# Optimization experiments

Hardware: AMD Instinct MI355X
Metric: run time of the kernel (lower is better)

Reference implementation:

```python
import jax, jax.numpy as jnp
import numpy as np

# model geometry (matches init_kwargs cfg)
D = 768        # D_EMB
PATCH = 16
T = 8192
N = T // PATCH # 512 patch tokens
H = 12         # heads
HD = D // H    # 64 head dim
NL = 6         # layers
DFF = 4 * D
B = 8
LN_EPS = 1e-5


def setup_inputs() -> dict:
    key = jax.random.key(0)
    ks = iter(jax.random.split(key, 32))
    def g(shape, scale=0.02):
        return jax.random.normal(next(ks), shape, jnp.float32) * scale
    return dict(
        x=jax.random.normal(next(ks), (B, T), jnp.float32),
        pp_w=g((D, PATCH)), pp_b=jnp.zeros((D,), jnp.float32),
        pe=g((N, D)),
        ln1_g=jnp.ones((NL, D), jnp.float32), ln1_b=jnp.zeros((NL, D), jnp.float32),
        qkv_w=g((NL, 3 * D, D)), out_w=g((NL, D, D)),
        ln2_g=jnp.ones((NL, D), jnp.float32), ln2_b=jnp.zeros((NL, D), jnp.float32),
        fc1_w=g((NL, DFF, D)), fc2_w=g((NL, D, DFF)),
        lnf_g=jnp.ones((D,), jnp.float32), lnf_b=jnp.zeros((D,), jnp.float32),
        h1_w=g((D // 2, D)), h1_b=jnp.zeros((D // 2,), jnp.float32),
        h2_w=g((2, D // 2)), h2_b=jnp.zeros((2,), jnp.float32),
    )


def _ln(x, g, b):
    m = x.mean(-1, keepdims=True)
    v = ((x - m) ** 2).mean(-1, keepdims=True)
    return (x - m) / jnp.sqrt(v + LN_EPS) * g + b


def reference(x, pp_w, pp_b, pe, ln1_g, ln1_b, qkv_w, out_w,
              ln2_g, ln2_b, fc1_w, fc2_w, lnf_g, lnf_b,
              h1_w, h1_b, h2_w, h2_b):
    Bx = x.shape[0]
    # patch embed: [B, N, PATCH] @ W^T + b -> [B, N, D]
    z = jnp.einsum('bnp,dp->bnd', x[:, :N * PATCH].reshape(Bx, N, PATCH), pp_w) + pp_b
    z = z + pe  # positional embedding (arange indexes whole table)
    mask = jnp.tril(jnp.ones((N, N), dtype=bool))
    for i in range(NL):
        # --- attention (manual causal softmax, dropout=eval/no-op) ---
        h = _ln(z, ln1_g[i], ln1_b[i])
        qkv = jnp.einsum('bnd,ed->bne', h, qkv_w[i])            # [B,N,3D]
        qkv = qkv.reshape(Bx, N, 3, H, HD).transpose(2, 0, 3, 1, 4)
        q, k, v = qkv[0], qkv[1], qkv[2]                         # [B,H,N,HD]
        s = jnp.einsum('bhld,bhmd->bhlm', q, k) / np.sqrt(HD)
        s = jnp.where(mask, s, -jnp.inf)
        a = jax.nn.softmax(s, axis=-1)
        o = jnp.einsum('bhlm,bhmd->bhld', a, v)
        o = o.transpose(0, 2, 1, 3).reshape(Bx, N, D)
        z = z + jnp.einsum('bnd,ed->bne', o, out_w[i])
        # --- FFN (exact gelu, matching F.gelu default) ---
        h = _ln(z, ln2_g[i], ln2_b[i])
        f = jax.nn.gelu(jnp.einsum('bnd,fd->bnf', h, fc1_w[i]), approximate=False)
        z = z + jnp.einsum('bnf,df->bnd', f, fc2_w[i])
    enc = _ln(z, lnf_g, lnf_b).mean(axis=1)                      # [B, D]
    y = jax.nn.relu(enc @ h1_w.T + h1_b)
    return y @ h2_w.T + h2_b                                     # [B, 2]
```

## Files before the change

kernel.cpp:

```cpp
#include <hip/hip_runtime.h>
#include <hip/hip_bf16.h>
#include <math.h>

#define D_EMB 768
#define NPATCH 16
#define NTOK 512
#define NHEAD 12
#define HDIM 64
#define NLAYER 6
#define DFF 3072
#define BATCH 8
#define MTOK (BATCH * NTOK)

typedef __attribute__((ext_vector_type(8))) short bf16x8;
typedef __attribute__((ext_vector_type(4))) float f32x4;

__device__ __forceinline__ float bf2f(ushort s) {
    unsigned u = ((unsigned)s) << 16;
    return __builtin_bit_cast(float, u);
}
__device__ __forceinline__ ushort f2bf(float f) {
    unsigned u = __builtin_bit_cast(unsigned, f);
    unsigned r = (u + 0x7FFFu + ((u >> 16) & 1u)) >> 16;
    return (ushort)r;
}

__global__ __launch_bounds__(256)
void f2bf_kernel(const float* __restrict__ in, ushort* __restrict__ out, int n4)
{
    int i = blockIdx.x * 256 + threadIdx.x;
    if (i >= n4) return;
    float4 v = *(const float4*)(in + (size_t)i * 4);
    ushort4 o;
    o.x = f2bf(v.x); o.y = f2bf(v.y); o.z = f2bf(v.z); o.w = f2bf(v.w);
    *(ushort4*)(out + (size_t)i * 4) = o;
}

__global__ __launch_bounds__(256)
void patch_embed_kernel(const float* __restrict__ x, const float* __restrict__ pw,
                        const float* __restrict__ pb, const float* __restrict__ pe,
                        float* __restrict__ z)
{
    int bn = blockIdx.x;
    int b = bn >> 9, n = bn & 511;
    __shared__ float xs[NPATCH];
    int t = threadIdx.x;
    if (t < NPATCH) xs[t] = x[(size_t)b * 8192 + n * NPATCH + t];
    __syncthreads();
    for (int d = t; d < D_EMB; d += 256) {
        float acc = pb[d] + pe[(size_t)n * D_EMB + d];
        const float* w = pw + (size_t)d * NPATCH;
        #pragma unroll
        for (int p = 0; p < NPATCH; ++p) acc += xs[p] * w[p];
        z[(size_t)bn * D_EMB + d] = acc;
    }
}

__device__ __forceinline__ float block_reduce_sum_256(float v)
{
    __shared__ float lds[4];
    #pragma unroll
    for (int o = 32; o > 0; o >>= 1) v += __shfl_xor(v, o);
    int lane = threadIdx.x & 63, wid = threadIdx.x >> 6;
    __syncthreads();
    if (lane == 0) lds[wid] = v;
    __syncthreads();
    return lds[0] + lds[1] + lds[2] + lds[3];
}

__device__ __forceinline__ void store_val(float* p, float v)  { *p = v; }
__device__ __forceinline__ void store_val(ushort* p, float v) { *p = f2bf(v); }

template<typename OT>
__global__ __launch_bounds__(256)
void ln_kernel(const float* __restrict__ x, const float* __restrict__ g,
               const float* __restrict__ bta, OT* __restrict__ y)
{
    int row = blockIdx.x;
    const float* xr = x + (size_t)row * D_EMB;
    int t = threadIdx.x;
    float vals[3];
    float s = 0.f;
    #pragma unroll
    for (int i = 0; i < 3; ++i) { vals[i] = xr[t + i * 256]; s += vals[i]; }
    float mean = block_reduce_sum_256(s) * (1.0f / D_EMB);
    float ss = 0.f;
    #pragma unroll
    for (int i = 0; i < 3; ++i) { float d = vals[i] - mean; ss += d * d; }
    float var = block_reduce_sum_256(ss) * (1.0f / D_EMB);
    float rstd = rsqrtf(var + 1e-5f);
    #pragma unroll
    for (int i = 0; i < 3; ++i) {
        int d = t + i * 256;
        store_val(y + (size_t)row * D_EMB + d, (vals[i] - mean) * rstd * g[d] + bta[d]);
    }
}

template<int EPI, typename OT>
__global__ __launch_bounds__(256)
void mfma_gemm(const ushort* __restrict__ A,
               const ushort* __restrict__ W,
               OT* __restrict__ C,
               const float* __restrict__ res,
               int N, int K)
{
    __shared__ ushort As[128 * 64];
    __shared__ ushort Bs[128 * 64];
    int bm = blockIdx.y * 128, bn = blockIdx.x * 128;
    int tid = threadIdx.x;
    int w = tid >> 6, l = tid & 63;
    int wr = w >> 1, wc = w & 1;
    int lr = l & 15, lg = l >> 4;
    f32x4 acc[4][4] = {};

    int srow = w * 32 + (l >> 3);
    int pcol = l & 7;

    for (int k0 = 0; k0 < K; k0 += 64) {
        #pragma unroll
        for (int j = 0; j < 4; ++j) {
            int row = srow + j * 8;
            int lcol = pcol ^ (row & 7);
            const ushort* sa = A + (size_t)(bm + row) * K + k0 + (lcol << 3);
            const ushort* sb = W + (size_t)(bn + row) * K + k0 + (lcol << 3);
            __builtin_amdgcn_global_load_lds(
                (const __attribute__((address_space(1))) unsigned int*)sa,
                (__attribute__((address_space(3))) unsigned int*)&As[row * 64 + (pcol << 3)],
                16, 0, 0);
            __builtin_amdgcn_global_load_lds(
                (const __attribute__((address_space(1))) unsigned int*)sb,
                (__attribute__((address_space(3))) unsigned int*)&Bs[row * 64 + (pcol << 3)],
                16, 0, 0);
        }
        __syncthreads();

        #pragma unroll
        for (int kk = 0; kk < 64; kk += 32) {
            int c = (kk >> 3) + lg;
            bf16x8 a[4], b[4];
            #pragma unroll
            for (int m = 0; m < 4; ++m) {
                int row = wr * 64 + m * 16 + lr;
                a[m] = *(const bf16x8*)(&As[row * 64 + ((c ^ (row & 7)) << 3)]);
            }
            #pragma unroll
            for (int n = 0; n < 4; ++n) {
                int row = wc * 64 + n * 16 + lr;
                b[n] = *(const bf16x8*)(&Bs[row * 64 + ((c ^ (row & 7)) << 3)]);
            }
            #pragma unroll
            for (int m = 0; m < 4; ++m)
                #pragma unroll
                for (int n = 0; n < 4; ++n)
                    acc[m][n] = __builtin_amdgcn_mfma_f32_16x16x32_bf16(a[m], b[n], acc[m][n], 0, 0, 0);
        }
        __syncthreads();
    }

    int r0 = lg * 4;
    #pragma unroll
    for (int m = 0; m < 4; ++m) {
        #pragma unroll
        for (int n = 0; n < 4; ++n) {
            #pragma unroll
            for (int j = 0; j < 4; ++j) {
                int gm = bm + wr * 64 + m * 16 + r0 + j;
                int gn = bn + wc * 64 + n * 16 + lr;
                float v = acc[m][n][j];
                if (EPI == 1) v = 0.5f * v * (1.0f + erff(v * 0.70710678118654752f));
                if (EPI == 2) v += res[(size_t)gm * N + gn];
                store_val(C + (size_t)gm * N + gn, v);
            }
        }
    }
}

__global__ __launch_bounds__(256)
void attn_mfma_kernel(const ushort* __restrict__ qkv, ushort* __restrict__ o)
{
    int w = threadIdx.x >> 6, l = threadIdx.x & 63;
    int qt = blockIdx.x * 4 + w;
    int h = blockIdx.y, b = blockIdx.z;
    int q0 = qt * 16;
    int lr = l & 15, lg = l >> 4;

    const size_t rs = 3 * D_EMB;
    const ushort* qbase = qkv + ((size_t)(b * NTOK)) * rs + h * HDIM;
    const ushort* kbase = qbase + D_EMB;
    const ushort* vbase = qbase + 2 * D_EMB;

    bf16x8 qf[2];
    qf[0] = *(const bf16x8*)(qbase + (size_t)(q0 + lr) * rs + lg * 8);
    qf[1] = *(const bf16x8*)(qbase + (size_t)(q0 + lr) * rs + 32 + lg * 8);

    f32x4 oacc[4] = {};
    float m_j[4], l_j[4];
    #pragma unroll
    for (int j = 0; j < 4; ++j) { m_j[j] = -1e30f; l_j[j] = 0.f; }

    __shared__ ushort P_lds[4][16][40];

    int ntiles = q0 / 32 + 1;
    for (int mt = 0; mt < ntiles; ++mt) {
        int m0 = mt * 32;
        f32x4 s[2] = {};
        #pragma unroll
        for (int kb = 0; kb < 2; ++kb) {
            const ushort* kr = kbase + (size_t)(m0 + kb * 16 + lr) * rs;
            bf16x8 k0 = *(const bf16x8*)(kr + lg * 8);
            bf16x8 k1 = *(const bf16x8*)(kr + 32 + lg * 8);
            s[kb] = __builtin_amdgcn_mfma_f32_16x16x32_bf16(qf[0], k0, s[kb], 0, 0, 0);
            s[kb] = __builtin_amdgcn_mfma_f32_16x16x32_bf16(qf[1], k1, s[kb], 0, 0, 0);
        }
        bool partial = (m0 + 31 > q0);
        float p[2][4], mx[4];
        #pragma unroll
        for (int j = 0; j < 4; ++j) {
            int qr = q0 + lg * 4 + j;
            float s0 = s[0][j] * 0.125f;
            float s1 = s[1][j] * 0.125f;
            if (partial) {
                if (m0 + lr > qr)      s0 = -1e30f;
                if (m0 + 16 + lr > qr) s1 = -1e30f;
            }
            p[0][j] = s0; p[1][j] = s1;
            float mm = fmaxf(s0, s1);
            mm = fmaxf(mm, __shfl_xor(mm, 1));
            mm = fmaxf(mm, __shfl_xor(mm, 2));
            mm = fmaxf(mm, __shfl_xor(mm, 4));
            mm = fmaxf(mm, __shfl_xor(mm, 8));
            mx[j] = mm;
        }
        #pragma unroll
        for (int j = 0; j < 4; ++j) {
            float mnew = fmaxf(m_j[j], mx[j]);
            float scale = __expf(m_j[j] - mnew);
            float p0 = __expf(p[0][j] - mnew);
            float p1 = __expf(p[1][j] - mnew);
            p[0][j] = p0; p[1][j] = p1;
            float rsum = p0 + p1;
            rsum += __shfl_xor(rsum, 1);
            rsum += __shfl_xor(rsum, 2);
            rsum += __shfl_xor(rsum, 4);
            rsum += __shfl_xor(rsum, 8);
            l_j[j] = l_j[j] * scale + rsum;
            m_j[j] = mnew;
            #pragma unroll
            for (int i = 0; i < 4; ++i) oacc[i][j] *= scale;
        }
        #pragma unroll
        for (int kb = 0; kb < 2; ++kb)
            #pragma unroll
            for (int j = 0; j < 4; ++j)
                P_lds[w][lg * 4 + j][kb * 16 + lr] = f2bf(p[kb][j]);
        asm volatile("s_waitcnt lgkmcnt(0)" ::: "memory");
        bf16x8 pa = *(const bf16x8*)(&P_lds[w][lr][lg * 8]);
        #pragma unroll
        for (int i = 0; i < 4; ++i) {
            bf16x8 vf;
            const ushort* vp = vbase + (size_t)(m0 + lg * 8) * rs + i * 16 + lr;
            #pragma unroll
            for (int j = 0; j < 8; ++j) vf[j] = (short)vp[(size_t)j * rs];
            oacc[i] = __builtin_amdgcn_mfma_f32_16x16x32_bf16(pa, vf, oacc[i], 0, 0, 0);
        }
    }
    #pragma unroll
    for (int i = 0; i < 4; ++i) {
        #pragma unroll
        for (int j = 0; j < 4; ++j) {
            int qr = q0 + lg * 4 + j;
            int d  = i * 16 + lr;
            float v = oacc[i][j] / l_j[j];
            o[((size_t)(b * NTOK + qr)) * D_EMB + h * HDIM + d] = f2bf(v);
        }
    }
}

__global__ void mean_kernel(const float* __restrict__ x, float* __restrict__ enc)
{
    int b = blockIdx.x; int d = threadIdx.x;
    float s = 0.f;
    for (int n = 0; n < NTOK; ++n) s += x[((size_t)(b * NTOK + n)) * D_EMB + d];
    enc[b * D_EMB + d] = s * (1.0f / NTOK);
}

__global__ void head1_kernel(const float* __restrict__ enc, const float* __restrict__ w,
                             const float* __restrict__ bias, float* __restrict__ r)
{
    int b = blockIdx.x; int j = threadIdx.x;
    float acc = bias[j];
    const float* e = enc + b * D_EMB;
    const float* wr = w + (size_t)j * D_EMB;
    for (int k = 0; k < D_EMB; ++k) acc += e[k] * wr[k];
    r[b * 384 + j] = fmaxf(acc, 0.f);
}

__global__ void head2_kernel(const float* __restrict__ r, const float* __restrict__ w,
                             const float* __restrict__ bias, float* __restrict__ out)
{
    int idx = threadIdx.x;
    if (idx >= 16) return;
    int b = idx >> 1, j = idx & 1;
    float acc = bias[j];
    for (int k = 0; k < 384; ++k) acc += r[b * 384 + k] * w[j * 384 + k];
    out[b * 2 + j] = acc;
}

extern "C" void kernel_launch(void* const* d_in, const int* in_sizes, int n_in,
                              void* d_out, int out_size, void* d_ws, size_t ws_size,
                              hipStream_t stream)
{
    const float* x     = (const float*)d_in[0];
    const float* pp_w  = (const float*)d_in[1];
    const float* pp_b  = (const float*)d_in[2];
    const float* pe    = (const float*)d_in[3];
    const float* ln1_g = (const float*)d_in[4];
    const float* ln1_b = (const float*)d_in[5];
    const float* qkv_w = (const float*)d_in[6];
    const float* out_w = (const float*)d_in[7];
    const float* ln2_g = (const float*)d_in[8];
    const float* ln2_b = (const float*)d_in[9];
    const float* fc1_w = (const float*)d_in[10];
    const float* fc2_w = (const float*)d_in[11];
    const float* lnf_g = (const float*)d_in[12];
    const float* lnf_b = (const float*)d_in[13];
    const float* h1_w  = (const float*)d_in[14];
    const float* h1_b  = (const float*)d_in[15];
    const float* h2_w  = (const float*)d_in[16];
    const float* h2_b  = (const float*)d_in[17];
    float* out = (float*)d_out;

    char* p = (char*)d_ws;
    float*  z      = (float*)p;  p += (size_t)MTOK * D_EMB * 4;
    ushort* big_bf = (ushort*)p; p += (size_t)MTOK * DFF * 2;
    ushort* h_bf   = (ushort*)p; p += (size_t)MTOK * D_EMB * 2;
    ushort* wq_bf  = (ushort*)p; p += (size_t)3 * D_EMB * D_EMB * 2;
    ushort* wo_bf  = (ushort*)p; p += (size_t)D_EMB * D_EMB * 2;
    ushort* wf1_bf = (ushort*)p; p += (size_t)DFF * D_EMB * 2;
    ushort* wf2_bf = (ushort*)p; p += (size_t)D_EMB * DFF * 2;
    float*  enc    = (float*)p;  p += BATCH * D_EMB * 4;
    float*  r1     = (float*)p;  p += BATCH * 384 * 4;
    float*  lnf_out = (float*)big_bf;

    patch_embed_kernel<<<MTOK, 256, 0, stream>>>(x, pp_w, pp_b, pe, z);

    const int nq = 3 * D_EMB * D_EMB, no = D_EMB * D_EMB, nf = DFF * D_EMB;

    for (int i = 0; i < NLAYER; ++i) {
        f2bf_kernel<<<(nq / 4 + 255) / 256, 256, 0, stream>>>(qkv_w + (size_t)i * nq, wq_bf, nq / 4);
        f2bf_kernel<<<(no / 4 + 255) / 256, 256, 0, stream>>>(out_w + (size_t)i * no, wo_bf, no / 4);
        f2bf_kernel<<<(nf / 4 + 255) / 256, 256, 0, stream>>>(fc1_w + (size_t)i * nf, wf1_bf, nf / 4);
        f2bf_kernel<<<(nf / 4 + 255) / 256, 256, 0, stream>>>(fc2_w + (size_t)i * nf, wf2_bf, nf / 4);

        ln_kernel<ushort><<<MTOK, 256, 0, stream>>>(z, ln1_g + i * D_EMB, ln1_b + i * D_EMB, h_bf);

        dim3 gq((3 * D_EMB) / 128, MTOK / 128);
        mfma_gemm<0, ushort><<<gq, 256, 0, stream>>>(h_bf, wq_bf, big_bf, nullptr, 3 * D_EMB, D_EMB);

        dim3 ga(NTOK / 64, NHEAD, BATCH);
        attn_mfma_kernel<<<ga, 256, 0, stream>>>(big_bf, h_bf);

        dim3 gp(D_EMB / 128, MTOK / 128);
        mfma_gemm<2, float><<<gp, 256, 0, stream>>>(h_bf, wo_bf, z, z, D_EMB, D_EMB);

        ln_kernel<ushort><<<MTOK, 256, 0, stream>>>(z, ln2_g + i * D_EMB, ln2_b + i * D_EMB, h_bf);

        dim3 g1(DFF / 128, MTOK / 128);
        mfma_gemm<1, ushort><<<g1, 256, 0, stream>>>(h_bf, wf1_bf, big_bf, nullptr, DFF, D_EMB);

        dim3 g2(D_EMB / 128, MTOK / 128);
        mfma_gemm<2, float><<<g2, 256, 0, stream>>>(big_bf, wf2_bf, z, z, D_EMB, DFF);
    }

    ln_kernel<float><<<MTOK, 256, 0, stream>>>(z, lnf_g, lnf_b, lnf_out);
    mean_kernel<<<BATCH, D_EMB, 0, stream>>>(lnf_out, enc);
    head1_kernel<<<BATCH, 384, 0, stream>>>(enc, h1_w, h1_b, r1);
    head2_kernel<<<1, 64, 0, stream>>>(r1, h2_w, h2_b, out);
}
```

Baseline: 1.293 ms.

## Double-buffer GEMM LDS tiles and remap blocks across XCDs

The MFMA GEMM now uses two LDS buffers per operand and issues the global-to-LDS load of the next K tile before computing on the current one, so memory latency can overlap with MFMA work. It also remaps block indices so that consecutive row-tiles land on the same XCD when the grid height is divisible by 8, improving L2 reuse of the A rows. LDS use doubles to 64 KB per block, which may reduce occupancy. The block remap changes which tiles share a cache.

```diff
diff --git a/kernel.cpp b/kernel.cpp
--- a/kernel.cpp
+++ b/kernel.cpp
@@ -104,9 +104,20 @@
                const float* __restrict__ res,
                int N, int K)
 {
-    __shared__ ushort As[128 * 64];
-    __shared__ ushort Bs[128 * 64];
-    int bm = blockIdx.y * 128, bn = blockIdx.x * 128;
+    __shared__ ushort As[2][128 * 64];
+    __shared__ ushort Bs[2][128 * 64];
+
+    int gx = gridDim.x, gy = gridDim.y;
+    int bx = blockIdx.x, by = blockIdx.y;
+    if ((gy & 7) == 0) {
+        int flat = by * gx + bx;
+        int xcd = flat & 7;
+        int j = flat >> 3;
+        by = xcd * (gy >> 3) + j / gx;
+        bx = j % gx;
+    }
+    int bm = by * 128, bn = bx * 128;
+
     int tid = threadIdx.x;
     int w = tid >> 6, l = tid & 63;
     int wr = w >> 1, wc = w & 1;
@@ -116,24 +127,46 @@
     int srow = w * 32 + (l >> 3);
     int pcol = l & 7;
 
-    for (int k0 = 0; k0 < K; k0 += 64) {
+    const int nk = K >> 6;
+    {
         #pragma unroll
         for (int j = 0; j < 4; ++j) {
             int row = srow + j * 8;
             int lcol = pcol ^ (row & 7);
-            const ushort* sa = A + (size_t)(bm + row) * K + k0 + (lcol << 3);
-            const ushort* sb = W + (size_t)(bn + row) * K + k0 + (lcol << 3);
+            const ushort* sa = A + (size_t)(bm + row) * K + (lcol << 3);
+            const ushort* sb = W + (size_t)(bn + row) * K + (lcol << 3);
             __builtin_amdgcn_global_load_lds(
                 (const __attribute__((address_space(1))) unsigned int*)sa,
-                (__attribute__((address_space(3))) unsigned int*)&As[row * 64 + (pcol << 3)],
+                (__attribute__((address_space(3))) unsigned int*)&As[0][row * 64 + (pcol << 3)],
                 16, 0, 0);
             __builtin_amdgcn_global_load_lds(
                 (const __attribute__((address_space(1))) unsigned int*)sb,
-                (__attribute__((address_space(3))) unsigned int*)&Bs[row * 64 + (pcol << 3)],
+                (__attribute__((address_space(3))) unsigned int*)&Bs[0][row * 64 + (pcol << 3)],
                 16, 0, 0);
         }
-        __syncthreads();
-
+    }
+    __syncthreads();
+
+    int cur = 0;
+    for (int t = 0; t < nk; ++t) {
+        if (t + 1 < nk) {
+            int k0 = (t + 1) << 6;
+            #pragma unroll
+            for (int j = 0; j < 4; ++j) {
+                int row = srow + j * 8;
+                int lcol = pcol ^ (row & 7);
+                const ushort* sa = A + (size_t)(bm + row) * K + k0 + (lcol << 3);
+                const ushort* sb = W + (size_t)(bn + row) * K + k0 + (lcol << 3);
+                __builtin_amdgcn_global_load_lds(
+                    (const __attribute__((address_space(1))) unsigned int*)sa,
+                    (__attribute__((address_space(3))) unsigned int*)&As[cur ^ 1][row * 64 + (pcol << 3)],
+                    16, 0, 0);
+                __builtin_amdgcn_global_load_lds(
+                    (const __attribute__((address_space(1))) unsigned int*)sb,
+                    (__attribute__((address_space(3))) unsigned int*)&Bs[cur ^ 1][row * 64 + (pcol << 3)],
+                    16, 0, 0);
+            }
+        }
         #pragma unroll
         for (int kk = 0; kk < 64; kk += 32) {
             int c = (kk >> 3) + lg;
@@ -141,12 +174,12 @@
             #pragma unroll
             for (int m = 0; m < 4; ++m) {
                 int row = wr * 64 + m * 16 + lr;
-                a[m] = *(const bf16x8*)(&As[row * 64 + ((c ^ (row & 7)) << 3)]);
+                a[m] = *(const bf16x8*)(&As[cur][row * 64 + ((c ^ (row & 7)) << 3)]);
             }
             #pragma unroll
             for (int n = 0; n < 4; ++n) {
                 int row = wc * 64 + n * 16 + lr;
-                b[n] = *(const bf16x8*)(&Bs[row * 64 + ((c ^ (row & 7)) << 3)]);
+                b[n] = *(const bf16x8*)(&Bs[cur][row * 64 + ((c ^ (row & 7)) << 3)]);
             }
             #pragma unroll
             for (int m = 0; m < 4; ++m)
@@ -155,6 +188,7 @@
                     acc[m][n] = __builtin_amdgcn_mfma_f32_16x16x32_bf16(a[m], b[n], acc[m][n], 0, 0, 0);
         }
         __syncthreads();
+        cur ^= 1;
     }
 
     int r0 = lg * 4;
```

After: 1.350 ms. 1.04x slower.

## Shrink GEMM tiles to 64x128, remap blocks per XCD, split-K the FC2 GEMM

Applied to the files above, without the earlier changes.

Changes the GEMM block tile from 128x128 to 64x128, with each wave computing a 64x32 slice, so the small-N projections launch more blocks and fill more CUs. Adds an XCD-aware block index remap so blocks sharing A rows land on the same XCD and can share its L2. The FC2 GEMM now uses split-K by 2, writing fp32 partials to a scratch buffer, and a separate reduce kernel adds the partials into the residual. The cost is lower per-block reuse, an extra kernel launch, and extra fp32 partial-sum traffic for FC2.

```diff
diff --git a/kernel.cpp b/kernel.cpp
--- a/kernel.cpp
+++ b/kernel.cpp
@@ -96,37 +96,59 @@
     }
 }
 
-template<int EPI, typename OT>
+template<int EPI, typename OT, bool SPLITK>
 __global__ __launch_bounds__(256)
 void mfma_gemm(const ushort* __restrict__ A,
                const ushort* __restrict__ W,
                OT* __restrict__ C,
                const float* __restrict__ res,
-               int N, int K)
-{
-    __shared__ ushort As[128 * 64];
+               int N, int K, int lda)
+{
+    __shared__ ushort As[64 * 64];
     __shared__ ushort Bs[128 * 64];
-    int bm = blockIdx.y * 128, bn = blockIdx.x * 128;
+
+    int gx = gridDim.x, gy = gridDim.y;
+    int bx = blockIdx.x, by = blockIdx.y;
+    int bz = SPLITK ? blockIdx.z : 0;
+    if ((gy & 7) == 0) {
+        int flat = bx + gx * (by + gy * bz);
+        int xcd = flat & 7, j = flat >> 3;
+        int ry = gy >> 3;
+        by = xcd * ry + (j % ry);
+        int rem = j / ry;
+        bx = rem % gx;
+        bz = rem / gx;
+    }
+    int bm = by * 64, bn = bx * 128;
+
+    const ushort* Ab = A + (size_t)bz * K;
+    const ushort* Wb = W + (size_t)bz * K;
+    OT* Cb = C + (size_t)bz * ((size_t)gy * 64) * N;
+
     int tid = threadIdx.x;
     int w = tid >> 6, l = tid & 63;
-    int wr = w >> 1, wc = w & 1;
     int lr = l & 15, lg = l >> 4;
-    f32x4 acc[4][4] = {};
-
-    int srow = w * 32 + (l >> 3);
+    f32x4 acc[4][2] = {};
+
+    int srow = w * 8 + (l >> 3);
     int pcol = l & 7;
 
     for (int k0 = 0; k0 < K; k0 += 64) {
         #pragma unroll
-        for (int j = 0; j < 4; ++j) {
-            int row = srow + j * 8;
+        for (int j = 0; j < 2; ++j) {
+            int row = j * 32 + srow;
             int lcol = pcol ^ (row & 7);
-            const ushort* sa = A + (size_t)(bm + row) * K + k0 + (lcol << 3);
-            const ushort* sb = W + (size_t)(bn + row) * K + k0 + (lcol << 3);
+            const ushort* sa = Ab + (size_t)(bm + row) * lda + k0 + (lcol << 3);
             __builtin_amdgcn_global_load_lds(
                 (const __attribute__((address_space(1))) unsigned int*)sa,
                 (__attribute__((address_space(3))) unsigned int*)&As[row * 64 + (pcol << 3)],
                 16, 0, 0);
+        }
+        #pragma unroll
+        for (int j = 0; j < 4; ++j) {
+            int row = j * 32 + srow;
+            int lcol = pcol ^ (row & 7);
+            const ushort* sb = Wb + (size_t)(bn + row) * lda + k0 + (lcol << 3);
             __builtin_amdgcn_global_load_lds(
                 (const __attribute__((address_space(1))) unsigned int*)sb,
                 (__attribute__((address_space(3))) unsigned int*)&Bs[row * 64 + (pcol << 3)],
@@ -137,21 +159,21 @@
         #pragma unroll
         for (int kk = 0; kk < 64; kk += 32) {
             int c = (kk >> 3) + lg;
-            bf16x8 a[4], b[4];
+            bf16x8 a[4], b[2];
             #pragma unroll
             for (int m = 0; m < 4; ++m) {
-                int row = wr * 64 + m * 16 + lr;
+                int row = m * 16 + lr;
                 a[m] = *(const bf16x8*)(&As[row * 64 + ((c ^ (row & 7)) << 3)]);
             }
             #pragma unroll
-            for (int n = 0; n < 4; ++n) {
-                int row = wc * 64 + n * 16 + lr;
+            for (int n = 0; n < 2; ++n) {
+                int row = w * 32 + n * 16 + lr;
                 b[n] = *(const bf16x8*)(&Bs[row * 64 + ((c ^ (row & 7)) << 3)]);
             }
             #pragma unroll
             for (int m = 0; m < 4; ++m)
                 #pragma unroll
-                for (int n = 0; n < 4; ++n)
+                for (int n = 0; n < 2; ++n)
                     acc[m][n] = __builtin_amdgcn_mfma_f32_16x16x32_bf16(a[m], b[n], acc[m][n], 0, 0, 0);
         }
         __syncthreads();
@@ -161,18 +183,30 @@
     #pragma unroll
     for (int m = 0; m < 4; ++m) {
         #pragma unroll
-        for (int n = 0; n < 4; ++n) {
+        for (int n = 0; n < 2; ++n) {
             #pragma unroll
             for (int j = 0; j < 4; ++j) {
-                int gm = bm + wr * 64 + m * 16 + r0 + j;
-                int gn = bn + wc * 64 + n * 16 + lr;
+                int gm = bm + m * 16 + r0 + j;
+                int gn = bn + w * 32 + n * 16 + lr;
                 float v = acc[m][n][j];
                 if (EPI == 1) v = 0.5f * v * (1.0f + erff(v * 0.70710678118654752f));
                 if (EPI == 2) v += res[(size_t)gm * N + gn];
-                store_val(C + (size_t)gm * N + gn, v);
+                store_val(Cb + (size_t)gm * N + gn, v);
             }
         }
     }
+}
+
+__global__ __launch_bounds__(256)
+void splitk_reduce(const float* __restrict__ p, float* __restrict__ z, int n4)
+{
+    int i = blockIdx.x * 256 + threadIdx.x;
+    if (i >= n4) return;
+    float4 a = ((const float4*)p)[i];
+    float4 b = ((const float4*)p)[i + (size_t)n4];
+    float4 c = ((float4*)z)[i];
+    c.x += a.x + b.x; c.y += a.y + b.y; c.z += a.z + b.z; c.w += a.w + b.w;
+    ((float4*)z)[i] = c;
 }
 
 __global__ __launch_bounds__(256)
@@ -338,6 +372,7 @@
     ushort* wo_bf  = (ushort*)p; p += (size_t)D_EMB * D_EMB * 2;
     ushort* wf1_bf = (ushort*)p; p += (size_t)DFF * D_EMB * 2;
     ushort* wf2_bf = (ushort*)p; p += (size_t)D_EMB * DFF * 2;
+    float*  pbuf   = (float*)p;  p += (size_t)2 * MTOK * D_EMB * 4;
     float*  enc    = (float*)p;  p += BATCH * D_EMB * 4;
     float*  r1     = (float*)p;  p += BATCH * 384 * 4;
     float*  lnf_out = (float*)big_bf;
@@ -345,6 +380,7 @@
     patch_embed_kernel<<<MTOK, 256, 0, stream>>>(x, pp_w, pp_b, pe, z);
 
     const int nq = 3 * D_EMB * D_EMB, no = D_EMB * D_EMB, nf = DFF * D_EMB;
+    const int n4red = MTOK * D_EMB / 4;
 
     for (int i = 0; i < NLAYER; ++i) {
         f2bf_kernel<<<(nq / 4 + 255) / 256, 256, 0, stream>>>(qkv_w + (size_t)i * nq, wq_bf, nq / 4);
@@ -354,22 +390,27 @@
 
         ln_kernel<ushort><<<MTOK, 256, 0, stream>>>(z, ln1_g + i * D_EMB, ln1_b + i * D_EMB, h_bf);
 
-        dim3 gq((3 * D_EMB) / 128, MTOK / 128);
-        mfma_gemm<0, ushort><<<gq, 256, 0, stream>>>(h_bf, wq_bf, big_bf, nullptr, 3 * D_EMB, D_EMB);
+        dim3 gq((3 * D_EMB) / 128, MTOK / 64);
+        mfma_gemm<0, ushort, false><<<gq, 256, 0, stream>>>(h_bf, wq_bf, big_bf, nullptr,
+                                                            3 * D_EMB, D_EMB, D_EMB);
 
         dim3 ga(NTOK / 64, NHEAD, BATCH);
         attn_mfma_kernel<<<ga, 256, 0, stream>>>(big_bf, h_bf);
 
-        dim3 gp(D_EMB / 128, MTOK / 128);
-        mfma_gemm<2, float><<<gp, 256, 0, stream>>>(h_bf, wo_bf, z, z, D_EMB, D_EMB);
+        dim3 gp(D_EMB / 128, MTOK / 64);
+        mfma_gemm<2, float, false><<<gp, 256, 0, stream>>>(h_bf, wo_bf, z, z,
+                                                           D_EMB, D_EMB, D_EMB);
 
         ln_kernel<ushort><<<MTOK, 256, 0, stream>>>(z, ln2_g + i * D_EMB, ln2_b + i * D_EMB, h_bf);
 
-        dim3 g1(DFF / 128, MTOK / 128);
-        mfma_gemm<1, ushort><<<g1, 256, 0, stream>>>(h_bf, wf1_bf, big_bf, nullptr, DFF, D_EMB);
-
-        dim3 g2(D_EMB / 128, MTOK / 128);
-        mfma_gemm<2, float><<<g2, 256, 0, stream>>>(big_bf, wf2_bf, z, z, D_EMB, DFF);
+        dim3 g1(DFF / 128, MTOK / 64);
+        mfma_gemm<1, ushort, false><<<g1, 256, 0, stream>>>(h_bf, wf1_bf, big_bf, nullptr,
+                                                            DFF, D_EMB, D_EMB);
+
+        dim3 g2(D_EMB / 128, MTOK / 64, 2);
+        mfma_gemm<0, float, true><<<g2, 256, 0, stream>>>(big_bf, wf2_bf, pbuf, nullptr,
+                                                          D_EMB, DFF / 2, DFF);
+        splitk_reduce<<<(n4red + 255) / 256, 256, 0, stream>>>(pbuf, z, n4red);
     }
 
     ln_kernel<float><<<MTOK, 256, 0, stream>>>(z, lnf_g, lnf_b, lnf_out);
```

New measurement: 1.129 ms. 1.14x faster.
